# Kernel optimization log

Measured on AMD Instinct MI355X. Metric: run time of the kernel, lower is better.

The kernel has to match this reference:

```python
import jax, jax.numpy as jnp
import numpy as np

N, K = 100000, 16
IN, H, OUT = 128, 256, 128
EPS = 1e-5
NEG_SLOPE = 0.2


def _bn(x, gamma, beta):
    # training-mode BatchNorm1d: biased batch stats over dim 0
    m = jnp.mean(x, axis=0)
    v = jnp.mean(jnp.square(x - m), axis=0)
    return (x - m) * jax.lax.rsqrt(v + EPS) * gamma + beta


def _layer(x, W, b, gamma, beta):
    x = x @ W.T + b
    x = jnp.where(x > 0, x, NEG_SLOPE * x)  # LeakyReLU(0.2)
    return _bn(x, gamma, beta)


def setup_inputs() -> dict:
    key = jax.random.key(0)
    ks = jax.random.split(key, 8)
    inp = {
        "input_features": jax.random.normal(ks[0], (N, IN), dtype=jnp.float32),
        "neigh_idx": jax.random.randint(ks[1], (N * K,), 0, N, dtype=jnp.int64 if jax.config.jax_enable_x64 else jnp.int32),
        "prob_retained": 1,
        "W1": jax.random.normal(ks[2], (H, IN), dtype=jnp.float32) * 0.05,
        "b1": jnp.zeros((H,), dtype=jnp.float32),
        "g1": jnp.ones((H,), dtype=jnp.float32),
        "beta1": jnp.zeros((H,), dtype=jnp.float32),
        "W2": jax.random.normal(ks[3], (H, H), dtype=jnp.float32) * 0.05,
        "b2": jnp.zeros((H,), dtype=jnp.float32),
        "g2": jnp.ones((H,), dtype=jnp.float32),
        "beta2": jnp.zeros((H,), dtype=jnp.float32),
        "W3": jax.random.normal(ks[4], (OUT, H), dtype=jnp.float32) * 0.05,
        "b3": jnp.zeros((OUT,), dtype=jnp.float32),
        "g3": jnp.ones((OUT,), dtype=jnp.float32),
        "beta3": jnp.zeros((OUT,), dtype=jnp.float32),
    }
    return inp


def reference(input_features, neigh_idx, prob_retained,
              W1, b1, g1, beta1, W2, b2, g2, beta2, W3, b3, g3, beta3):
    # MLP (BN branch, len(x) > 1)
    f = _layer(input_features, W1, b1, g1, beta1)   # [N, H]
    f = _layer(f, W2, b2, g2, beta2)                # [N, H]
    f = _layer(f, W3, b3, g3, beta3)                # [N, OUT]
    # per-node neighbor mean: index_select + mean, fixed degree K
    node_update = f[neigh_idx].reshape(N, K, OUT).mean(axis=1)  # [N, OUT]
    return (node_update, f)
```

## Files before the change

### kernel.cpp

```cpp
#include <hip/hip_runtime.h>
#include <hip/hip_bf16.h>

typedef __bf16 bf16x8 __attribute__((ext_vector_type(8)));
typedef __bf16 bf16x2 __attribute__((ext_vector_type(2)));
typedef float f32x4 __attribute__((ext_vector_type(4)));

#define NROWS 100000
#define NSTRIPS 6250
#define EPS 1e-5f
#define SLOPE 0.2f

__device__ __forceinline__ bf16x8 cvt8(const float* s) {
    float4 x0 = *(const float4*)s, x1 = *(const float4*)(s + 4);
    bf16x8 o;
    o[0] = (__bf16)x0.x; o[1] = (__bf16)x0.y; o[2] = (__bf16)x0.z; o[3] = (__bf16)x0.w;
    o[4] = (__bf16)x1.x; o[5] = (__bf16)x1.y; o[6] = (__bf16)x1.z; o[7] = (__bf16)x1.w;
    return o;
}

template <int KT, int NI, bool F32IN>
__global__ __launch_bounds__(256, 2)
void gemm_stream(const __bf16* __restrict__ A, const float* __restrict__ A32,
                 const __bf16* __restrict__ W, const float* __restrict__ W32,
                 const float* __restrict__ bias, __bf16* __restrict__ Y,
                 float* __restrict__ sum, float* __restrict__ sumsq)
{
    constexpr int KS = KT / 32;
    constexpr int NCOLS = NI * 64;
    const int wave = threadIdx.x >> 6, lane = threadIdx.x & 63;
    const int quad = lane >> 4, l16 = lane & 15;
    const int c0 = wave * (NI * 16);

    bf16x8 bfrag[NI][KS];
    float bcol[NI];
    #pragma unroll
    for (int ni = 0; ni < NI; ++ni) {
        int col = c0 + ni * 16 + l16;
        bcol[ni] = bias[col];
        #pragma unroll
        for (int ks = 0; ks < KS; ++ks) {
            int k = ks * 32 + quad * 8;
            if constexpr (F32IN) bfrag[ni][ks] = cvt8(W32 + (size_t)col * KT + k);
            else                 bfrag[ni][ks] = *(const bf16x8*)(W + (size_t)col * KT + k);
        }
    }

    float csum[NI] = {}, csq[NI] = {};

    for (int s = blockIdx.x; s < NSTRIPS; s += gridDim.x) {
        int row0 = s * 16;
        bf16x8 afrag[KS];
        #pragma unroll
        for (int ks = 0; ks < KS; ++ks) {
            int k = ks * 32 + quad * 8;
            if constexpr (F32IN) afrag[ks] = cvt8(A32 + (size_t)(row0 + l16) * KT + k);
            else                 afrag[ks] = *(const bf16x8*)(A + (size_t)(row0 + l16) * KT + k);
        }
        f32x4 acc[NI] = {};
        #pragma unroll
        for (int ks = 0; ks < KS; ++ks)
            #pragma unroll
            for (int ni = 0; ni < NI; ++ni)
                acc[ni] = __builtin_amdgcn_mfma_f32_16x16x32_bf16(
                    afrag[ks], bfrag[ni][ks], acc[ni], 0, 0, 0);

        #pragma unroll
        for (int ni = 0; ni < NI; ++ni) {
            int col = c0 + ni * 16 + l16;
            #pragma unroll
            for (int r = 0; r < 4; ++r) {
                float y = acc[ni][r] + bcol[ni];
                y = (y > 0.f) ? y : SLOPE * y;
                Y[(size_t)(row0 + quad * 4 + r) * NCOLS + col] = (__bf16)y;
                csum[ni] += y;
                csq[ni]  += y * y;
            }
        }
    }

    #pragma unroll
    for (int ni = 0; ni < NI; ++ni) {
        float s = csum[ni], q = csq[ni];
        s += __shfl_xor(s, 16); s += __shfl_xor(s, 32);
        q += __shfl_xor(q, 16); q += __shfl_xor(q, 32);
        if (quad == 0) {
            int col = c0 + ni * 16 + l16;
            atomicAdd(&sum[col], s);
            atomicAdd(&sumsq[col], q);
        }
    }
}

__global__ void stats_k(const float* __restrict__ sum, const float* __restrict__ sumsq,
                        const float* __restrict__ g, const float* __restrict__ beta,
                        float* __restrict__ s, float* __restrict__ t,
                        int Ncols, float invN)
{
    int c = blockIdx.x * blockDim.x + threadIdx.x;
    if (c < Ncols) {
        float m = sum[c] * invN;
        float v = sumsq[c] * invN - m * m;
        float sc = g[c] * rsqrtf(v + EPS);
        s[c] = sc;
        t[c] = beta[c] - m * sc;
    }
}

__global__ void fold_k(const float* __restrict__ W, const float* __restrict__ b,
                       const float* __restrict__ s, const float* __restrict__ t,
                       __bf16* __restrict__ Wf, float* __restrict__ bf_, int K)
{
    int n = blockIdx.x;
    int lane = threadIdx.x;
    float dot = 0.f;
    for (int k = lane; k < K; k += 64) {
        float w = W[(size_t)n * K + k];
        Wf[(size_t)n * K + k] = (__bf16)(w * s[k]);
        dot += w * t[k];
    }
    #pragma unroll
    for (int off = 32; off; off >>= 1) dot += __shfl_down(dot, off);
    if (lane == 0) bf_[n] = b[n] + dot;
}

__global__ void bn_apply(const __bf16* __restrict__ Y, const float* __restrict__ s,
                         const float* __restrict__ t, float* __restrict__ F, long n8)
{
    long i = blockIdx.x * (long)blockDim.x + threadIdx.x;
    if (i >= n8) return;
    bf16x8 v = *(const bf16x8*)(Y + i * 8);
    int c0 = (int)((i * 8) & 127);
    float4 f0, f1;
    f0.x = (float)v[0] * s[c0 + 0] + t[c0 + 0];
    f0.y = (float)v[1] * s[c0 + 1] + t[c0 + 1];
    f0.z = (float)v[2] * s[c0 + 2] + t[c0 + 2];
    f0.w = (float)v[3] * s[c0 + 3] + t[c0 + 3];
    f1.x = (float)v[4] * s[c0 + 4] + t[c0 + 4];
    f1.y = (float)v[5] * s[c0 + 5] + t[c0 + 5];
    f1.z = (float)v[6] * s[c0 + 6] + t[c0 + 6];
    f1.w = (float)v[7] * s[c0 + 7] + t[c0 + 7];
    *(float4*)(F + i * 8) = f0;
    *(float4*)(F + i * 8 + 4) = f1;
}

__global__ __launch_bounds__(256)
void gather_mean_bn(const __bf16* __restrict__ Y3, const int* __restrict__ idx,
                    const float* __restrict__ s3, const float* __restrict__ t3,
                    float* __restrict__ out, int N)
{
    int row = blockIdx.x * 4 + (threadIdx.x >> 6);
    if (row >= N) return;
    int lane = threadIdx.x & 63;
    const int* ib = idx + (size_t)row * 16;
    float a0 = 0.f, a1 = 0.f;
    #pragma unroll
    for (int k = 0; k < 16; ++k) {
        int j = ib[k];
        bf16x2 v = *(const bf16x2*)(Y3 + (size_t)j * 128 + lane * 2);
        a0 += (float)v[0];
        a1 += (float)v[1];
    }
    float2 sc = *(const float2*)(s3 + lane * 2);
    float2 tc = *(const float2*)(t3 + lane * 2);
    float2 o;
    o.x = a0 * 0.0625f * sc.x + tc.x;
    o.y = a1 * 0.0625f * sc.y + tc.y;
    *(float2*)(out + (size_t)row * 128 + lane * 2) = o;
}

extern "C" void kernel_launch(void* const* d_in, const int* in_sizes, int n_in,
                              void* d_out, int out_size, void* d_ws, size_t ws_size,
                              hipStream_t stream)
{
    const float* X   = (const float*)d_in[0];
    const int*   idx = (const int*)d_in[1];
    const float* W1  = (const float*)d_in[3];
    const float* b1  = (const float*)d_in[4];
    const float* g1  = (const float*)d_in[5];
    const float* be1 = (const float*)d_in[6];
    const float* W2  = (const float*)d_in[7];
    const float* b2  = (const float*)d_in[8];
    const float* g2  = (const float*)d_in[9];
    const float* be2 = (const float*)d_in[10];
    const float* W3  = (const float*)d_in[11];
    const float* b3  = (const float*)d_in[12];
    const float* g3  = (const float*)d_in[13];
    const float* be3 = (const float*)d_in[14];

    char* ws = (char*)d_ws;
    float* sum1 = (float*)(ws + 0);
    float* sq1  = (float*)(ws + 1024);
    float* sum2 = (float*)(ws + 2048);
    float* sq2  = (float*)(ws + 3072);
    float* sum3 = (float*)(ws + 4096);
    float* sq3  = (float*)(ws + 4608);
    float* s1   = (float*)(ws + 5120);
    float* t1   = (float*)(ws + 6144);
    float* s2   = (float*)(ws + 7168);
    float* t2   = (float*)(ws + 8192);
    float* s3   = (float*)(ws + 9216);
    float* t3   = (float*)(ws + 9728);
    float* b2f  = (float*)(ws + 10240);
    float* b3f  = (float*)(ws + 11264);
    __bf16* W2f = (__bf16*)(ws + 13312);
    __bf16* W3f = (__bf16*)(ws + 144384);
    __bf16* Y1  = (__bf16*)(ws + (1 << 20));
    __bf16* Y2  = (__bf16*)(ws + (1 << 20) + 51200000);
    __bf16* Y3  = Y1;

    float* out_nu = (float*)d_out;
    float* F      = out_nu + (size_t)NROWS * 128;

    const float invN = 1.0f / (float)NROWS;
    const dim3 blk(256);
    const int GB = 512;

    hipMemsetAsync(d_ws, 0, 5120, stream);

    gemm_stream<128, 4, true><<<GB, blk, 0, stream>>>(
        nullptr, X, nullptr, W1, b1, Y1, sum1, sq1);
    stats_k<<<1, 256, 0, stream>>>(sum1, sq1, g1, be1, s1, t1, 256, invN);
    fold_k<<<256, 64, 0, stream>>>(W2, b2, s1, t1, W2f, b2f, 256);

    gemm_stream<256, 4, false><<<GB, blk, 0, stream>>>(
        Y1, nullptr, W2f, nullptr, b2f, Y2, sum2, sq2);
    stats_k<<<1, 256, 0, stream>>>(sum2, sq2, g2, be2, s2, t2, 256, invN);
    fold_k<<<128, 64, 0, stream>>>(W3, b3, s2, t2, W3f, b3f, 256);

    gemm_stream<256, 2, false><<<GB, blk, 0, stream>>>(
        Y2, nullptr, W3f, nullptr, b3f, Y3, sum3, sq3);
    stats_k<<<1, 128, 0, stream>>>(sum3, sq3, g3, be3, s3, t3, 128, invN);

    bn_apply<<<6250, 256, 0, stream>>>(Y3, s3, t3, F, (long)NROWS * 128 / 8);
    gather_mean_bn<<<25000, 256, 0, stream>>>(Y3, idx, s3, t3, out_nu, NROWS);
}
```

Before: 365.7 us.

## Pipeline GEMM strip loads, transpose MFMA output, fuse stats/fold and BN-apply into gather

The streaming GEMM now double-buffers A-strip loads in registers so the next strip's global loads overlap the current strip's MFMAs. Operands are swapped so each lane holds four consecutive columns, which allows vectorized bf16x4 stores and per-lane float4 bias and stat accumulation. Layers 2 and 3 now use 8-wave blocks with fewer columns per wave. The stats kernel is folded into the weight-fold kernel, and the separate BN-apply pass is fused into the gather-mean kernel, which removes several launches and one full read of Y3. The cost is more registers from double buffering and redundant stats computation in every block.

```diff
diff --git a/kernel.cpp b/kernel.cpp
--- a/kernel.cpp
+++ b/kernel.cpp
@@ -2,6 +2,7 @@
 #include <hip/hip_bf16.h>
 
 typedef __bf16 bf16x8 __attribute__((ext_vector_type(8)));
+typedef __bf16 bf16x4 __attribute__((ext_vector_type(4)));
 typedef __bf16 bf16x2 __attribute__((ext_vector_type(2)));
 typedef float f32x4 __attribute__((ext_vector_type(4)));
 
@@ -9,163 +10,204 @@
 #define NSTRIPS 6250
 #define EPS 1e-5f
 #define SLOPE 0.2f
-
-__device__ __forceinline__ bf16x8 cvt8(const float* s) {
-    float4 x0 = *(const float4*)s, x1 = *(const float4*)(s + 4);
+#define INVN 1e-5f
+
+__device__ __forceinline__ bf16x8 cvt8(float4 x0, float4 x1) {
     bf16x8 o;
     o[0] = (__bf16)x0.x; o[1] = (__bf16)x0.y; o[2] = (__bf16)x0.z; o[3] = (__bf16)x0.w;
     o[4] = (__bf16)x1.x; o[5] = (__bf16)x1.y; o[6] = (__bf16)x1.z; o[7] = (__bf16)x1.w;
     return o;
 }
 
-template <int KT, int NI, bool F32IN>
-__global__ __launch_bounds__(256, 2)
+template <int KT, int NI, int WAVES, bool F32IN>
+__global__ __launch_bounds__(WAVES * 64, 2)
 void gemm_stream(const __bf16* __restrict__ A, const float* __restrict__ A32,
                  const __bf16* __restrict__ W, const float* __restrict__ W32,
                  const float* __restrict__ bias, __bf16* __restrict__ Y,
                  float* __restrict__ sum, float* __restrict__ sumsq)
 {
     constexpr int KS = KT / 32;
-    constexpr int NCOLS = NI * 64;
+    constexpr int NCOLS = NI * 16 * WAVES;
     const int wave = threadIdx.x >> 6, lane = threadIdx.x & 63;
     const int quad = lane >> 4, l16 = lane & 15;
     const int c0 = wave * (NI * 16);
 
     bf16x8 bfrag[NI][KS];
-    float bcol[NI];
+    f32x4 bias4[NI];
     #pragma unroll
     for (int ni = 0; ni < NI; ++ni) {
-        int col = c0 + ni * 16 + l16;
-        bcol[ni] = bias[col];
+        const int colb = c0 + ni * 16;
+        const float4 b4 = *(const float4*)(bias + colb + quad * 4);
+        bias4[ni][0] = b4.x; bias4[ni][1] = b4.y; bias4[ni][2] = b4.z; bias4[ni][3] = b4.w;
+        const int col = colb + l16;
         #pragma unroll
         for (int ks = 0; ks < KS; ++ks) {
-            int k = ks * 32 + quad * 8;
-            if constexpr (F32IN) bfrag[ni][ks] = cvt8(W32 + (size_t)col * KT + k);
-            else                 bfrag[ni][ks] = *(const bf16x8*)(W + (size_t)col * KT + k);
-        }
-    }
-
-    float csum[NI] = {}, csq[NI] = {};
-
-    for (int s = blockIdx.x; s < NSTRIPS; s += gridDim.x) {
-        int row0 = s * 16;
-        bf16x8 afrag[KS];
-        #pragma unroll
-        for (int ks = 0; ks < KS; ++ks) {
-            int k = ks * 32 + quad * 8;
-            if constexpr (F32IN) afrag[ks] = cvt8(A32 + (size_t)(row0 + l16) * KT + k);
-            else                 afrag[ks] = *(const bf16x8*)(A + (size_t)(row0 + l16) * KT + k);
-        }
-        f32x4 acc[NI] = {};
-        #pragma unroll
-        for (int ks = 0; ks < KS; ++ks)
-            #pragma unroll
-            for (int ni = 0; ni < NI; ++ni)
-                acc[ni] = __builtin_amdgcn_mfma_f32_16x16x32_bf16(
-                    afrag[ks], bfrag[ni][ks], acc[ni], 0, 0, 0);
-
-        #pragma unroll
-        for (int ni = 0; ni < NI; ++ni) {
-            int col = c0 + ni * 16 + l16;
-            #pragma unroll
-            for (int r = 0; r < 4; ++r) {
-                float y = acc[ni][r] + bcol[ni];
-                y = (y > 0.f) ? y : SLOPE * y;
-                Y[(size_t)(row0 + quad * 4 + r) * NCOLS + col] = (__bf16)y;
-                csum[ni] += y;
-                csq[ni]  += y * y;
+            const int k = ks * 32 + quad * 8;
+            if constexpr (F32IN) {
+                const float* p = W32 + (size_t)col * KT + k;
+                bfrag[ni][ks] = cvt8(*(const float4*)p, *(const float4*)(p + 4));
+            } else {
+                bfrag[ni][ks] = *(const bf16x8*)(W + (size_t)col * KT + k);
             }
         }
     }
 
+    f32x4 csum[NI] = {}, csq[NI] = {};
+    float4 rawf[2][KS][2];
+    bf16x8 rawb[2][KS];
+
+#define LOAD_STRIP(BUF, S) do {                                                   \
+        const int row_ = (S) * 16 + l16;                                          \
+        _Pragma("unroll")                                                         \
+        for (int ks = 0; ks < KS; ++ks) {                                         \
+            const int k_ = ks * 32 + quad * 8;                                    \
+            if constexpr (F32IN) {                                                \
+                const float* p_ = A32 + (size_t)row_ * KT + k_;                   \
+                rawf[BUF][ks][0] = *(const float4*)p_;                            \
+                rawf[BUF][ks][1] = *(const float4*)(p_ + 4);                      \
+            } else {                                                              \
+                rawb[BUF][ks] = *(const bf16x8*)(A + (size_t)row_ * KT + k_);     \
+            }                                                                     \
+        }                                                                         \
+    } while (0)
+
+#define COMPUTE_STORE(BUF, S) do {                                                \
+        bf16x8 af_[KS];                                                           \
+        _Pragma("unroll")                                                         \
+        for (int ks = 0; ks < KS; ++ks) {                                         \
+            if constexpr (F32IN) af_[ks] = cvt8(rawf[BUF][ks][0], rawf[BUF][ks][1]); \
+            else                 af_[ks] = rawb[BUF][ks];                         \
+        }                                                                         \
+        f32x4 acc_[NI] = {};                                                      \
+        _Pragma("unroll")                                                         \
+        for (int ks = 0; ks < KS; ++ks)                                           \
+            _Pragma("unroll")                                                     \
+            for (int ni = 0; ni < NI; ++ni)                                       \
+                acc_[ni] = __builtin_amdgcn_mfma_f32_16x16x32_bf16(               \
+                    bfrag[ni][ks], af_[ks], acc_[ni], 0, 0, 0);                   \
+        const int row_ = (S) * 16 + l16;                                          \
+        __bf16* yp_ = Y + (size_t)row_ * NCOLS + c0 + quad * 4;                   \
+        _Pragma("unroll")                                                         \
+        for (int ni = 0; ni < NI; ++ni) {                                         \
+            f32x4 y_;                                                             \
+            _Pragma("unroll")                                                     \
+            for (int r = 0; r < 4; ++r) {                                         \
+                float v_ = acc_[ni][r] + bias4[ni][r];                            \
+                v_ = (v_ > 0.f) ? v_ : SLOPE * v_;                                \
+                y_[r] = v_;                                                       \
+            }                                                                     \
+            csum[ni] += y_;                                                       \
+            csq[ni]  += y_ * y_;                                                  \
+            bf16x4 o_;                                                            \
+            o_[0] = (__bf16)y_[0]; o_[1] = (__bf16)y_[1];                         \
+            o_[2] = (__bf16)y_[2]; o_[3] = (__bf16)y_[3];                         \
+            *(bf16x4*)(yp_ + ni * 16) = o_;                                       \
+        }                                                                         \
+    } while (0)
+
+    int s = blockIdx.x;
+    const int stride = gridDim.x;
+    if (s < NSTRIPS) {
+        LOAD_STRIP(0, s);
+        while (true) {
+            int sn = s + stride;
+            if (sn < NSTRIPS) LOAD_STRIP(1, sn);
+            COMPUTE_STORE(0, s);
+            s = sn;
+            if (s >= NSTRIPS) break;
+            sn = s + stride;
+            if (sn < NSTRIPS) LOAD_STRIP(0, sn);
+            COMPUTE_STORE(1, s);
+            s = sn;
+            if (s >= NSTRIPS) break;
+        }
+    }
+#undef LOAD_STRIP
+#undef COMPUTE_STORE
+
     #pragma unroll
     for (int ni = 0; ni < NI; ++ni) {
-        float s = csum[ni], q = csq[ni];
-        s += __shfl_xor(s, 16); s += __shfl_xor(s, 32);
-        q += __shfl_xor(q, 16); q += __shfl_xor(q, 32);
-        if (quad == 0) {
-            int col = c0 + ni * 16 + l16;
-            atomicAdd(&sum[col], s);
-            atomicAdd(&sumsq[col], q);
+        #pragma unroll
+        for (int r = 0; r < 4; ++r) {
+            float sv = csum[ni][r], qv = csq[ni][r];
+            sv += __shfl_xor(sv, 1);  qv += __shfl_xor(qv, 1);
+            sv += __shfl_xor(sv, 2);  qv += __shfl_xor(qv, 2);
+            sv += __shfl_xor(sv, 4);  qv += __shfl_xor(qv, 4);
+            sv += __shfl_xor(sv, 8);  qv += __shfl_xor(qv, 8);
+            if (l16 == 0) {
+                const int col = c0 + ni * 16 + quad * 4 + r;
+                atomicAdd(&sum[col], sv);
+                atomicAdd(&sumsq[col], qv);
+            }
         }
     }
 }
 
-__global__ void stats_k(const float* __restrict__ sum, const float* __restrict__ sumsq,
-                        const float* __restrict__ g, const float* __restrict__ beta,
-                        float* __restrict__ s, float* __restrict__ t,
-                        int Ncols, float invN)
-{
-    int c = blockIdx.x * blockDim.x + threadIdx.x;
-    if (c < Ncols) {
-        float m = sum[c] * invN;
-        float v = sumsq[c] * invN - m * m;
-        float sc = g[c] * rsqrtf(v + EPS);
-        s[c] = sc;
-        t[c] = beta[c] - m * sc;
-    }
-}
-
-__global__ void fold_k(const float* __restrict__ W, const float* __restrict__ b,
-                       const float* __restrict__ s, const float* __restrict__ t,
-                       __bf16* __restrict__ Wf, float* __restrict__ bf_, int K)
-{
-    int n = blockIdx.x;
-    int lane = threadIdx.x;
+__global__ void fold_stats_k(const float* __restrict__ sum, const float* __restrict__ sumsq,
+                             const float* __restrict__ g, const float* __restrict__ beta,
+                             const float* __restrict__ W, const float* __restrict__ b,
+                             __bf16* __restrict__ Wf, float* __restrict__ bf_, int K)
+{
+    __shared__ float s_sh[256], t_sh[256];
+    const int n = blockIdx.x, lane = threadIdx.x;
+    for (int k = lane; k < K; k += 64) {
+        float m = sum[k] * INVN;
+        float v = sumsq[k] * INVN - m * m;
+        float sc = g[k] * rsqrtf(v + EPS);
+        s_sh[k] = sc;
+        t_sh[k] = beta[k] - m * sc;
+    }
+    __syncthreads();
     float dot = 0.f;
     for (int k = lane; k < K; k += 64) {
         float w = W[(size_t)n * K + k];
-        Wf[(size_t)n * K + k] = (__bf16)(w * s[k]);
-        dot += w * t[k];
+        Wf[(size_t)n * K + k] = (__bf16)(w * s_sh[k]);
+        dot += w * t_sh[k];
     }
     #pragma unroll
     for (int off = 32; off; off >>= 1) dot += __shfl_down(dot, off);
     if (lane == 0) bf_[n] = b[n] + dot;
 }
 
-__global__ void bn_apply(const __bf16* __restrict__ Y, const float* __restrict__ s,
-                         const float* __restrict__ t, float* __restrict__ F, long n8)
-{
-    long i = blockIdx.x * (long)blockDim.x + threadIdx.x;
-    if (i >= n8) return;
-    bf16x8 v = *(const bf16x8*)(Y + i * 8);
-    int c0 = (int)((i * 8) & 127);
-    float4 f0, f1;
-    f0.x = (float)v[0] * s[c0 + 0] + t[c0 + 0];
-    f0.y = (float)v[1] * s[c0 + 1] + t[c0 + 1];
-    f0.z = (float)v[2] * s[c0 + 2] + t[c0 + 2];
-    f0.w = (float)v[3] * s[c0 + 3] + t[c0 + 3];
-    f1.x = (float)v[4] * s[c0 + 4] + t[c0 + 4];
-    f1.y = (float)v[5] * s[c0 + 5] + t[c0 + 5];
-    f1.z = (float)v[6] * s[c0 + 6] + t[c0 + 6];
-    f1.w = (float)v[7] * s[c0 + 7] + t[c0 + 7];
-    *(float4*)(F + i * 8) = f0;
-    *(float4*)(F + i * 8 + 4) = f1;
-}
-
 __global__ __launch_bounds__(256)
-void gather_mean_bn(const __bf16* __restrict__ Y3, const int* __restrict__ idx,
-                    const float* __restrict__ s3, const float* __restrict__ t3,
-                    float* __restrict__ out, int N)
-{
-    int row = blockIdx.x * 4 + (threadIdx.x >> 6);
+void finalize_k(const __bf16* __restrict__ Y3, const int* __restrict__ idx,
+                const float* __restrict__ sum3, const float* __restrict__ sq3,
+                const float* __restrict__ g3, const float* __restrict__ be3,
+                float* __restrict__ F, float* __restrict__ out, int N)
+{
+    const int row = blockIdx.x * 4 + (threadIdx.x >> 6);
     if (row >= N) return;
-    int lane = threadIdx.x & 63;
+    const int lane = threadIdx.x & 63;
+    const int c = lane * 2;
+
+    const float2 sm = *(const float2*)(sum3 + c);
+    const float2 sq = *(const float2*)(sq3 + c);
+    const float2 gg = *(const float2*)(g3 + c);
+    const float2 bb = *(const float2*)(be3 + c);
+    const float m0 = sm.x * INVN, m1 = sm.y * INVN;
+    const float v0 = sq.x * INVN - m0 * m0, v1 = sq.y * INVN - m1 * m1;
+    const float s0 = gg.x * rsqrtf(v0 + EPS), s1 = gg.y * rsqrtf(v1 + EPS);
+    const float t0 = bb.x - m0 * s0, t1 = bb.y - m1 * s1;
+
+    bf16x2 own = *(const bf16x2*)(Y3 + (size_t)row * 128 + c);
+    float2 f;
+    f.x = (float)own[0] * s0 + t0;
+    f.y = (float)own[1] * s1 + t1;
+    *(float2*)(F + (size_t)row * 128 + c) = f;
+
     const int* ib = idx + (size_t)row * 16;
     float a0 = 0.f, a1 = 0.f;
     #pragma unroll
     for (int k = 0; k < 16; ++k) {
-        int j = ib[k];
-        bf16x2 v = *(const bf16x2*)(Y3 + (size_t)j * 128 + lane * 2);
+        const int j = ib[k];
+        bf16x2 v = *(const bf16x2*)(Y3 + (size_t)j * 128 + c);
         a0 += (float)v[0];
         a1 += (float)v[1];
     }
-    float2 sc = *(const float2*)(s3 + lane * 2);
-    float2 tc = *(const float2*)(t3 + lane * 2);
     float2 o;
-    o.x = a0 * 0.0625f * sc.x + tc.x;
-    o.y = a1 * 0.0625f * sc.y + tc.y;
-    *(float2*)(out + (size_t)row * 128 + lane * 2) = o;
+    o.x = a0 * 0.0625f * s0 + t0;
+    o.y = a1 * 0.0625f * s1 + t1;
+    *(float2*)(out + (size_t)row * 128 + c) = o;
 }
 
 extern "C" void kernel_launch(void* const* d_in, const int* in_sizes, int n_in,
@@ -194,12 +236,6 @@
     float* sq2  = (float*)(ws + 3072);
     float* sum3 = (float*)(ws + 4096);
     float* sq3  = (float*)(ws + 4608);
-    float* s1   = (float*)(ws + 5120);
-    float* t1   = (float*)(ws + 6144);
-    float* s2   = (float*)(ws + 7168);
-    float* t2   = (float*)(ws + 8192);
-    float* s3   = (float*)(ws + 9216);
-    float* t3   = (float*)(ws + 9728);
     float* b2f  = (float*)(ws + 10240);
     float* b3f  = (float*)(ws + 11264);
     __bf16* W2f = (__bf16*)(ws + 13312);
@@ -211,26 +247,18 @@
     float* out_nu = (float*)d_out;
     float* F      = out_nu + (size_t)NROWS * 128;
 
-    const float invN = 1.0f / (float)NROWS;
-    const dim3 blk(256);
-    const int GB = 512;
-
     hipMemsetAsync(d_ws, 0, 5120, stream);
 
-    gemm_stream<128, 4, true><<<GB, blk, 0, stream>>>(
+    gemm_stream<128, 4, 4, true><<<512, 256, 0, stream>>>(
         nullptr, X, nullptr, W1, b1, Y1, sum1, sq1);
-    stats_k<<<1, 256, 0, stream>>>(sum1, sq1, g1, be1, s1, t1, 256, invN);
-    fold_k<<<256, 64, 0, stream>>>(W2, b2, s1, t1, W2f, b2f, 256);
-
-    gemm_stream<256, 4, false><<<GB, blk, 0, stream>>>(
+    fold_stats_k<<<256, 64, 0, stream>>>(sum1, sq1, g1, be1, W2, b2, W2f, b2f, 256);
+
+    gemm_stream<256, 2, 8, false><<<256, 512, 0, stream>>>(
         Y1, nullptr, W2f, nullptr, b2f, Y2, sum2, sq2);
-    stats_k<<<1, 256, 0, stream>>>(sum2, sq2, g2, be2, s2, t2, 256, invN);
-    fold_k<<<128, 64, 0, stream>>>(W3, b3, s2, t2, W3f, b3f, 256);
-
-    gemm_stream<256, 2, false><<<GB, blk, 0, stream>>>(
+    fold_stats_k<<<128, 64, 0, stream>>>(sum2, sq2, g2, be2, W3, b3, W3f, b3f, 256);
+
+    gemm_stream<256, 1, 8, false><<<256, 512, 0, stream>>>(
         Y2, nullptr, W3f, nullptr, b3f, Y3, sum3, sq3);
-    stats_k<<<1, 128, 0, stream>>>(sum3, sq3, g3, be3, s3, t3, 128, invN);
-
-    bn_apply<<<6250, 256, 0, stream>>>(Y3, s3, t3, F, (long)NROWS * 128 / 8);
-    gather_mean_bn<<<25000, 256, 0, stream>>>(Y3, idx, s3, t3, out_nu, NROWS);
-}
+
+    finalize_k<<<25000, 256, 0, stream>>>(Y3, idx, sum3, sq3, g3, be3, F, out_nu, NROWS);
+}
```

After: 456.4 us. 1.25x slower.

## Fuse BN stats into fold/finalize kernels and retune GEMM wave layout

Applied to the files above, without the earlier changes.

The stats kernels are merged into the weight-fold kernel and into a combined finalize kernel, which applies BN to each row and computes the neighbor mean in one pass. This removes three small launches and the separate bn_apply pass over Y3. The GEMMs are templated on wave count and occupancy: layer 1 uses 1536 blocks with min 6 waves per EU, and layers 2-3 use 8-wave blocks with fewer columns per wave, so each wave holds fewer B fragments. Each fold block now recomputes the stats redundantly, and the finalize kernel recomputes scale and shift per row.

```diff
diff --git a/kernel.cpp b/kernel.cpp
--- a/kernel.cpp
+++ b/kernel.cpp
@@ -9,6 +9,7 @@
 #define NSTRIPS 6250
 #define EPS 1e-5f
 #define SLOPE 0.2f
+#define INVN 1e-5f
 
 __device__ __forceinline__ bf16x8 cvt8(const float* s) {
     float4 x0 = *(const float4*)s, x1 = *(const float4*)(s + 4);
@@ -18,15 +19,15 @@
     return o;
 }
 
-template <int KT, int NI, bool F32IN>
-__global__ __launch_bounds__(256, 2)
+template <int KT, int NI, int WAVES, int MINW, bool F32IN>
+__global__ __launch_bounds__(WAVES * 64, MINW)
 void gemm_stream(const __bf16* __restrict__ A, const float* __restrict__ A32,
                  const __bf16* __restrict__ W, const float* __restrict__ W32,
                  const float* __restrict__ bias, __bf16* __restrict__ Y,
                  float* __restrict__ sum, float* __restrict__ sumsq)
 {
     constexpr int KS = KT / 32;
-    constexpr int NCOLS = NI * 64;
+    constexpr int NCOLS = NI * 16 * WAVES;
     const int wave = threadIdx.x >> 6, lane = threadIdx.x & 63;
     const int quad = lane >> 4, l16 = lane & 15;
     const int c0 = wave * (NI * 16);
@@ -91,81 +92,71 @@
     }
 }
 
-__global__ void stats_k(const float* __restrict__ sum, const float* __restrict__ sumsq,
-                        const float* __restrict__ g, const float* __restrict__ beta,
-                        float* __restrict__ s, float* __restrict__ t,
-                        int Ncols, float invN)
-{
-    int c = blockIdx.x * blockDim.x + threadIdx.x;
-    if (c < Ncols) {
-        float m = sum[c] * invN;
-        float v = sumsq[c] * invN - m * m;
-        float sc = g[c] * rsqrtf(v + EPS);
-        s[c] = sc;
-        t[c] = beta[c] - m * sc;
-    }
-}
-
-__global__ void fold_k(const float* __restrict__ W, const float* __restrict__ b,
-                       const float* __restrict__ s, const float* __restrict__ t,
-                       __bf16* __restrict__ Wf, float* __restrict__ bf_, int K)
-{
-    int n = blockIdx.x;
-    int lane = threadIdx.x;
+__global__ void fold_stats_k(const float* __restrict__ sum, const float* __restrict__ sumsq,
+                             const float* __restrict__ g, const float* __restrict__ beta,
+                             const float* __restrict__ W, const float* __restrict__ b,
+                             __bf16* __restrict__ Wf, float* __restrict__ bf_, int K)
+{
+    __shared__ float s_sh[256], t_sh[256];
+    const int n = blockIdx.x, lane = threadIdx.x;
+    for (int k = lane; k < K; k += 64) {
+        float m = sum[k] * INVN;
+        float v = sumsq[k] * INVN - m * m;
+        float sc = g[k] * rsqrtf(v + EPS);
+        s_sh[k] = sc;
+        t_sh[k] = beta[k] - m * sc;
+    }
+    __syncthreads();
     float dot = 0.f;
     for (int k = lane; k < K; k += 64) {
         float w = W[(size_t)n * K + k];
-        Wf[(size_t)n * K + k] = (__bf16)(w * s[k]);
-        dot += w * t[k];
+        Wf[(size_t)n * K + k] = (__bf16)(w * s_sh[k]);
+        dot += w * t_sh[k];
     }
     #pragma unroll
     for (int off = 32; off; off >>= 1) dot += __shfl_down(dot, off);
     if (lane == 0) bf_[n] = b[n] + dot;
 }
 
-__global__ void bn_apply(const __bf16* __restrict__ Y, const float* __restrict__ s,
-                         const float* __restrict__ t, float* __restrict__ F, long n8)
-{
-    long i = blockIdx.x * (long)blockDim.x + threadIdx.x;
-    if (i >= n8) return;
-    bf16x8 v = *(const bf16x8*)(Y + i * 8);
-    int c0 = (int)((i * 8) & 127);
-    float4 f0, f1;
-    f0.x = (float)v[0] * s[c0 + 0] + t[c0 + 0];
-    f0.y = (float)v[1] * s[c0 + 1] + t[c0 + 1];
-    f0.z = (float)v[2] * s[c0 + 2] + t[c0 + 2];
-    f0.w = (float)v[3] * s[c0 + 3] + t[c0 + 3];
-    f1.x = (float)v[4] * s[c0 + 4] + t[c0 + 4];
-    f1.y = (float)v[5] * s[c0 + 5] + t[c0 + 5];
-    f1.z = (float)v[6] * s[c0 + 6] + t[c0 + 6];
-    f1.w = (float)v[7] * s[c0 + 7] + t[c0 + 7];
-    *(float4*)(F + i * 8) = f0;
-    *(float4*)(F + i * 8 + 4) = f1;
-}
-
 __global__ __launch_bounds__(256)
-void gather_mean_bn(const __bf16* __restrict__ Y3, const int* __restrict__ idx,
-                    const float* __restrict__ s3, const float* __restrict__ t3,
-                    float* __restrict__ out, int N)
-{
-    int row = blockIdx.x * 4 + (threadIdx.x >> 6);
+void finalize_k(const __bf16* __restrict__ Y3, const int* __restrict__ idx,
+                const float* __restrict__ sum3, const float* __restrict__ sq3,
+                const float* __restrict__ g3, const float* __restrict__ be3,
+                float* __restrict__ F, float* __restrict__ out, int N)
+{
+    const int row = blockIdx.x * 4 + (threadIdx.x >> 6);
     if (row >= N) return;
-    int lane = threadIdx.x & 63;
+    const int lane = threadIdx.x & 63;
+    const int c = lane * 2;
+
+    const float2 sm = *(const float2*)(sum3 + c);
+    const float2 sq = *(const float2*)(sq3 + c);
+    const float2 gg = *(const float2*)(g3 + c);
+    const float2 bb = *(const float2*)(be3 + c);
+    const float m0 = sm.x * INVN, m1 = sm.y * INVN;
+    const float v0 = sq.x * INVN - m0 * m0, v1 = sq.y * INVN - m1 * m1;
+    const float s0 = gg.x * rsqrtf(v0 + EPS), s1 = gg.y * rsqrtf(v1 + EPS);
+    const float t0 = bb.x - m0 * s0, t1 = bb.y - m1 * s1;
+
+    bf16x2 own = *(const bf16x2*)(Y3 + (size_t)row * 128 + c);
+    float2 f;
+    f.x = (float)own[0] * s0 + t0;
+    f.y = (float)own[1] * s1 + t1;
+    *(float2*)(F + (size_t)row * 128 + c) = f;
+
     const int* ib = idx + (size_t)row * 16;
     float a0 = 0.f, a1 = 0.f;
     #pragma unroll
     for (int k = 0; k < 16; ++k) {
-        int j = ib[k];
-        bf16x2 v = *(const bf16x2*)(Y3 + (size_t)j * 128 + lane * 2);
+        const int j = ib[k];
+        bf16x2 v = *(const bf16x2*)(Y3 + (size_t)j * 128 + c);
         a0 += (float)v[0];
         a1 += (float)v[1];
     }
-    float2 sc = *(const float2*)(s3 + lane * 2);
-    float2 tc = *(const float2*)(t3 + lane * 2);
     float2 o;
-    o.x = a0 * 0.0625f * sc.x + tc.x;
-    o.y = a1 * 0.0625f * sc.y + tc.y;
-    *(float2*)(out + (size_t)row * 128 + lane * 2) = o;
+    o.x = a0 * 0.0625f * s0 + t0;
+    o.y = a1 * 0.0625f * s1 + t1;
+    *(float2*)(out + (size_t)row * 128 + c) = o;
 }
 
 extern "C" void kernel_launch(void* const* d_in, const int* in_sizes, int n_in,
@@ -194,12 +185,6 @@
     float* sq2  = (float*)(ws + 3072);
     float* sum3 = (float*)(ws + 4096);
     float* sq3  = (float*)(ws + 4608);
-    float* s1   = (float*)(ws + 5120);
-    float* t1   = (float*)(ws + 6144);
-    float* s2   = (float*)(ws + 7168);
-    float* t2   = (float*)(ws + 8192);
-    float* s3   = (float*)(ws + 9216);
-    float* t3   = (float*)(ws + 9728);
     float* b2f  = (float*)(ws + 10240);
     float* b3f  = (float*)(ws + 11264);
     __bf16* W2f = (__bf16*)(ws + 13312);
@@ -211,26 +196,18 @@
     float* out_nu = (float*)d_out;
     float* F      = out_nu + (size_t)NROWS * 128;
 
-    const float invN = 1.0f / (float)NROWS;
-    const dim3 blk(256);
-    const int GB = 512;
-
     hipMemsetAsync(d_ws, 0, 5120, stream);
 
-    gemm_stream<128, 4, true><<<GB, blk, 0, stream>>>(
+    gemm_stream<128, 4, 4, 6, true><<<1536, 256, 0, stream>>>(
         nullptr, X, nullptr, W1, b1, Y1, sum1, sq1);
-    stats_k<<<1, 256, 0, stream>>>(sum1, sq1, g1, be1, s1, t1, 256, invN);
-    fold_k<<<256, 64, 0, stream>>>(W2, b2, s1, t1, W2f, b2f, 256);
-
-    gemm_stream<256, 4, false><<<GB, blk, 0, stream>>>(
+    fold_stats_k<<<256, 64, 0, stream>>>(sum1, sq1, g1, be1, W2, b2, W2f, b2f, 256);
+
+    gemm_stream<256, 2, 8, 4, false><<<512, 512, 0, stream>>>(
         Y1, nullptr, W2f, nullptr, b2f, Y2, sum2, sq2);
-    stats_k<<<1, 256, 0, stream>>>(sum2, sq2, g2, be2, s2, t2, 256, invN);
-    fold_k<<<128, 64, 0, stream>>>(W3, b3, s2, t2, W3f, b3f, 256);
-
-    gemm_stream<256, 2, false><<<GB, blk, 0, stream>>>(
+    fold_stats_k<<<128, 64, 0, stream>>>(sum2, sq2, g2, be2, W3, b3, W3f, b3f, 256);
+
+    gemm_stream<256, 1, 8, 4, false><<<512, 512, 0, stream>>>(
         Y2, nullptr, W3f, nullptr, b3f, Y3, sum3, sq3);
-    stats_k<<<1, 128, 0, stream>>>(sum3, sq3, g3, be3, s3, t3, 128, invN);
-
-    bn_apply<<<6250, 256, 0, stream>>>(Y3, s3, t3, F, (long)NROWS * 128 / 8);
-    gather_mean_bn<<<25000, 256, 0, stream>>>(Y3, idx, s3, t3, out_nu, NROWS);
-}
+
+    finalize_k<<<25000, 256, 0, stream>>>(Y3, idx, sum3, sq3, g3, be3, F, out_nu, NROWS);
+}
```

Measured after the change: 457.0 us. 25.0% more time.
